# Performance work log

Hardware: AMD Instinct MI355X
Metric: run time of the kernel (lower is better)

Reference implementation:

```python
import jax, jax.numpy as jnp
import numpy as np

D_MODEL = 2048
NUM_GROUPS = 16
D_HEAD = D_MODEL // NUM_GROUPS
ROTARY_DIM = int(D_MODEL * 0.25)  # 512


def setup_inputs() -> dict:
    key = jax.random.key(0)
    ks = jax.random.split(key, 8)
    B, S, N = 4, 2048, 2048
    scale = 1.0 / np.sqrt(D_MODEL)
    return {
        "query": jax.random.normal(ks[0], (B, S, D_MODEL), jnp.float32),
        "key": jax.random.normal(ks[1], (B, N, D_MODEL), jnp.float32),
        "value": jax.random.normal(ks[2], (B, N, D_MODEL), jnp.float32),
        "mask": jax.random.randint(ks[3], (B, S), 0, 2, jnp.int32),
        "position_ids": jnp.arange(S, dtype=jnp.int64) if jax.config.jax_enable_x64 else jnp.arange(S, dtype=jnp.int32),
        "Wq": jax.random.normal(ks[4], (D_MODEL, D_MODEL), jnp.float32) * scale,
        "Wk": jax.random.normal(ks[5], (D_MODEL, D_MODEL), jnp.float32) * scale,
        "Wv": jax.random.normal(ks[6], (D_MODEL, D_MODEL), jnp.float32) * scale,
        "Wo": jax.random.normal(ks[7], (D_MODEL, D_MODEL), jnp.float32) * scale,
    }


def _apply_rope_query_only(q, k, position_ids):
    # Faithful to source: rotary embedding is applied to query ONLY; key is returned unchanged.
    rd = ROTARY_DIM
    pos = position_ids.astype(q.dtype)  # (S,)
    freq = jnp.arange(0, rd, 2, dtype=q.dtype)
    inv_freq = 1.0 / (10000.0 ** (freq / rd))  # (rd/2,)
    pe = pos[:, None] * inv_freq[None, :]       # (S, rd/2)
    cos = jnp.tile(jnp.cos(pe), (1, 2))[None]   # (1, S, rd) tiled [c, c]
    sin = jnp.tile(jnp.sin(pe), (1, 2))[None]
    q_rot, q_pass = q[..., :rd], q[..., rd:]
    half = rd // 2
    q_rot_half = jnp.concatenate([-q_rot[..., half:], q_rot[..., :half]], axis=-1)
    q_rot = q_rot * cos + q_rot_half * sin
    q = jnp.concatenate([q_rot, q_pass], axis=-1)
    return q, k


def reference(query, key, value, mask, position_ids, Wq, Wk, Wv, Wo):
    B, S, _ = query.shape
    N = key.shape[1]
    G, dh = NUM_GROUPS, D_HEAD

    q = query @ Wq.T
    k = key @ Wk.T
    v = value @ Wv.T

    q, k = _apply_rope_query_only(q, k, position_ids)

    qh = q.reshape(B, S, G, dh).transpose(0, 2, 1, 3)  # (B,G,S,dh)
    kh = k.reshape(B, N, G, dh).transpose(0, 2, 1, 3)  # (B,G,N,dh)
    vh = v.reshape(B, N, G, dh).transpose(0, 2, 1, 3)  # (B,G,N,dh)

    scores = jnp.einsum("bgsd,bgnd->bgsn", qh, kh) / jnp.sqrt(jnp.asarray(dh, q.dtype))
    # mask (B,S) -> (B,1,1,N); here S == N so pad width is 0 (pad value 1 in source)
    m = mask[:, None, None, :]
    scores = jnp.where(m == 0, -jnp.inf, scores)

    w = jax.nn.softmax(scores, axis=-1)
    out = jnp.einsum("bgsn,bgnd->bgsd", w, vh)           # (B,G,S,dh)
    out = out.transpose(0, 2, 1, 3).reshape(B, S, D_MODEL)
    return out @ Wo.T
```

## Files before the change

### kernel.cpp

```cpp
#include <hip/hip_runtime.h>
#include <hip/hip_bf16.h>
#include <type_traits>
#include <utility>

typedef unsigned short u16;
typedef unsigned int u32;
typedef __attribute__((ext_vector_type(8))) short  s16x8;
typedef __attribute__((ext_vector_type(4))) short  s16x4;
typedef __attribute__((ext_vector_type(4))) float  f32x4;
typedef __attribute__((ext_vector_type(16))) float f32x16;
typedef __bf16 bf16x8_t __attribute__((ext_vector_type(8)));
typedef __bf16 bf16x2_t __attribute__((ext_vector_type(2)));

#define SEQ 2048
#define DMODEL 2048
#define NBATCH 4
#define DH 128
#define NB (NBATCH * SEQ)

#define QK_SCALE_LOG2 0.12754375f
#define BIAS_VALID  (-34.624681f)
#define BIAS_MASKED (-180.0f)

#if __has_builtin(__builtin_amdgcn_exp2f)
#define EXP2(x) __builtin_amdgcn_exp2f(x)
#else
#define EXP2(x) exp2f(x)
#endif

#define BARRIER __builtin_amdgcn_s_barrier()
#define LGKM0  asm volatile("s_waitcnt lgkmcnt(0)" ::: "memory")
#define VMCNT4 asm volatile("s_waitcnt vmcnt(4)" ::: "memory")
#define VMCNT0 asm volatile("s_waitcnt vmcnt(0)" ::: "memory")

static __device__ __forceinline__ u16 f2bf(float f) {
  unsigned u = __float_as_uint(f);
  u += 0x7fffu + ((u >> 16) & 1u);
  return (u16)(u >> 16);
}
static __device__ __forceinline__ float bf2f(u16 h) {
  return __uint_as_float(((unsigned)h) << 16);
}
static __device__ __forceinline__ u32 pack_bf16(float a, float b) {
  bf16x2_t t; t[0] = (__bf16)a; t[1] = (__bf16)b;
  return __builtin_bit_cast(u32, t);
}
static __device__ __forceinline__ void plswap(u32& a, u32& b) {
  asm("v_permlane32_swap_b32 %0, %1" : "+v"(a), "+v"(b));
}

template <typename T, typename = void>
struct mfma_takes : std::false_type {};
template <typename T>
struct mfma_takes<T, std::void_t<decltype(__builtin_amdgcn_mfma_f32_16x16x32_bf16(
    std::declval<T>(), std::declval<T>(), std::declval<f32x4>(), 0, 0, 0))>>
    : std::true_type {};
using mfma_frag_t = std::conditional_t<mfma_takes<s16x8>::value, s16x8, bf16x8_t>;

static __device__ __forceinline__ f32x16 mfma32(s16x8 a, s16x8 b, f32x16 c) {
  return __builtin_amdgcn_mfma_f32_32x32x16_bf16(
      __builtin_bit_cast(mfma_frag_t, a), __builtin_bit_cast(mfma_frag_t, b), c, 0, 0, 0);
}

typedef const void __attribute__((address_space(1)))* gas_ptr;
typedef void __attribute__((address_space(3)))* las_ptr;
static __device__ __forceinline__ void gload16(const void* g, void* l) {
  __builtin_amdgcn_global_load_lds((gas_ptr)g, (las_ptr)l, 16, 0, 0);
}

static __device__ __forceinline__ s16x8 frag_from_words(u32 w0, u32 w1, u32 w2, u32 w3) {
  union { u32 w[4]; s16x8 v; } u;
  u.w[0] = w0; u.w[1] = w1; u.w[2] = w2; u.w[3] = w3;
  return u.v;
}

static __device__ __forceinline__ void cvt8(const float* src, u16* dst, int i) {
  const float4* p = (const float4*)src + (size_t)i * 2;
  float4 a = p[0], b4 = p[1];
  s16x8 o;
  o[0] = (short)f2bf(a.x);  o[1] = (short)f2bf(a.y);
  o[2] = (short)f2bf(a.z);  o[3] = (short)f2bf(a.w);
  o[4] = (short)f2bf(b4.x); o[5] = (short)f2bf(b4.y);
  o[6] = (short)f2bf(b4.z); o[7] = (short)f2bf(b4.w);
  *(s16x8*)(dst + (size_t)i * 8) = o;
}

__global__ void cvtall_k(const float* __restrict__ q, const float* __restrict__ a,
                         const float* __restrict__ b, const float* __restrict__ c,
                         const float* __restrict__ d, u16* __restrict__ oq,
                         u16* __restrict__ oa, u16* __restrict__ ob,
                         u16* __restrict__ oc, u16* __restrict__ od) {
  const int nq = 1 << 21, nw = 1 << 19;
  const int total = nq + 4 * nw;
  const int stride = (int)(gridDim.x * blockDim.x);
  for (int i = (int)(blockIdx.x * blockDim.x + threadIdx.x); i < total; i += stride) {
    if (i < nq) {
      cvt8(q, oq, i);
    } else {
      const int j = i - nq;
      const int seg = j >> 19, off = j & (nw - 1);
      const float* src = seg == 0 ? a : (seg == 1 ? b : (seg == 2 ? c : d));
      u16* dst = seg == 0 ? oa : (seg == 1 ? ob : (seg == 2 ? oc : od));
      cvt8(src, dst, off);
    }
  }
}

__global__ void scan_k(const int* __restrict__ mask, int* __restrict__ idx,
                       u16* __restrict__ biasc, int* __restrict__ meta) {
  __shared__ int nv_sh[4];
  const int tid = (int)threadIdx.x;
  const int w = tid >> 6, lane = tid & 63;
  const int* mb = mask + w * SEQ;
  int cnt = 0;
  for (int it = 0; it < SEQ / 64; ++it) {
    const int i = it * 64 + lane;
    const bool m = mb[i] != 0;
    const unsigned long long bal = __ballot(m);
    const int pos = cnt + __popcll(bal & ((1ull << lane) - 1ull));
    if (m) idx[w * SEQ + pos] = i;
    cnt += __popcll(bal);
  }
  if (lane == 0) nv_sh[w] = cnt;
  __syncthreads();
  const int nv = nv_sh[w];
  const int npad = (nv + 255) & ~255;
  for (int j = nv + lane; j < npad; j += 64) idx[w * SEQ + j] = 0;
  for (int j = lane; j < SEQ; j += 64)
    biasc[w * SEQ + j] = (j < nv) ? f2bf(BIAS_VALID) : f2bf(BIAS_MASKED);
  if (tid == 0) {
    int off = 0;
    for (int b2 = 0; b2 < 4; ++b2) {
      const int nvb = nv_sh[b2];
      meta[b2] = off;
      meta[4 + b2] = (nvb + 63) >> 6;
      off += (nvb + 255) & ~255;
    }
    meta[8] = off;
  }
}

__global__ void gathercvt_k(const float* __restrict__ keyf,
                            const float* __restrict__ valf,
                            const int* __restrict__ idx, const int* __restrict__ meta,
                            u16* __restrict__ xkc, u16* __restrict__ xvc) {
  const int b = (int)blockIdx.y;
  const int j = (int)blockIdx.x;
  const int mstart = meta[b];
  const int mend = (b < 3) ? meta[b + 1] : meta[8];
  if (mstart + j >= mend) return;
  const int src = idx[b * SEQ + j];
  const float* ks = keyf + ((size_t)b * SEQ + src) * DMODEL;
  const float* vs = valf + ((size_t)b * SEQ + src) * DMODEL;
  u16* kd = xkc + (size_t)(mstart + j) * DMODEL;
  u16* vd = xvc + (size_t)(mstart + j) * DMODEL;
  cvt8(ks, kd, (int)threadIdx.x);
  cvt8(vs, vd, (int)threadIdx.x);
}

static __device__ void gemm_body(const u16* __restrict__ A, const u16* __restrict__ Bw,
                                 void* __restrict__ Cv, const int outmode,
                                 const int bm, const int bn, const int mlimit) {
  constexpr int M = 8192, N = 2048, K = 2048;
  constexpr int NT = K / 64;
  __shared__ u16 Ab[2][256 * 64];
  __shared__ u16 Bb[2][256 * 64];

  if (bm * 256 >= mlimit) return;

  const int tid = (int)threadIdx.x;
  const int wv = tid >> 6, lane = tid & 63;
  const int l32 = lane & 31, hi = lane >> 5;
  const int wm = wv >> 2, wn = wv & 3;

  const size_t arow0 = (size_t)bm * 256;
  const size_t brow0 = (size_t)bn * 256;

  const int srow = tid >> 3;
  const int scolb = (tid & 7) * 16;
  const int scol = (scolb ^ ((srow & 7) << 4)) >> 1;
  const u16* agp = A  + (arow0 + srow) * (size_t)K + scol;
  const u16* bgp = Bw + (brow0 + srow) * (size_t)K + scol;

  f32x16 acc[4][2];
#pragma unroll
  for (int mi = 0; mi < 4; ++mi)
#pragma unroll
    for (int ni = 0; ni < 2; ++ni)
#pragma unroll
      for (int r = 0; r < 16; ++r) acc[mi][ni][r] = 0.f;

  auto SH_A = [&](int kt2, u16* bufA, int half) {
#pragma unroll
    for (int j = 0; j < 2; ++j) {
      const int rb = half * 128 + j * 64;
      gload16(agp + (size_t)rb * K + kt2, bufA + (rb + wv * 8) * 64);
    }
  };
  auto SH_B = [&](int kt2, u16* bufB, int half) {
#pragma unroll
    for (int j = 0; j < 2; ++j) {
      const int rb = half * 128 + j * 64;
      gload16(bgp + (size_t)rb * K + kt2, bufB + (rb + wv * 8) * 64);
    }
  };
  auto LDA = [&](const u16* buf, int qm, s16x8* af) {
#pragma unroll
    for (int mb = 0; mb < 2; ++mb) {
      const int row = wm * 128 + qm * 64 + mb * 32 + l32;
#pragma unroll
      for (int ks = 0; ks < 4; ++ks) {
        const int cb = ((ks * 32 + hi * 16) ^ ((row & 7) << 4)) >> 1;
        af[mb * 4 + ks] = *(const s16x8*)&buf[row * 64 + cb];
      }
    }
  };
  auto LDB = [&](const u16* buf, int qn, s16x8* bfr) {
    const int row = wn * 64 + qn * 32 + l32;
#pragma unroll
    for (int ks = 0; ks < 4; ++ks) {
      const int cb = ((ks * 32 + hi * 16) ^ ((row & 7) << 4)) >> 1;
      bfr[ks] = *(const s16x8*)&buf[row * 64 + cb];
    }
  };
  auto MM = [&](const s16x8* af, const s16x8* bfr, int qm, int qn) {
    __builtin_amdgcn_s_setprio(1);
#pragma unroll
    for (int mb = 0; mb < 2; ++mb)
#pragma unroll
      for (int ks = 0; ks < 4; ++ks)
        acc[qm * 2 + mb][qn] = mfma32(af[mb * 4 + ks], bfr[ks], acc[qm * 2 + mb][qn]);
    __builtin_amdgcn_s_setprio(0);
  };

  SH_A(0, Ab[0], 0); SH_A(0, Ab[0], 1);
  SH_B(0, Bb[0], 0); SH_B(0, Bb[0], 1);
  SH_B(64, Bb[1], 0); SH_B(64, Bb[1], 1);
  VMCNT4; BARRIER;

  for (int t = 0; t < NT; ++t) {
    u16* Ac = Ab[t & 1];
    u16* Bc = Bb[t & 1];
    u16* An = Ab[(t + 1) & 1];
    u16* Bn = Bb[t & 1];
    const int kA = (t + 1) * 64;
    const int kB = (t + 2) * 64;
    const bool stA = (t + 1 < NT);
    const bool stB = (t + 2 < NT);
    s16x8 af0[8], af1[8], bf0[4], bf1[4];

    LDA(Ac, 0, af0); LDB(Bc, 0, bf0);
    if (stA) SH_A(kA, An, 0);
    BARRIER; LGKM0;
    MM(af0, bf0, 0, 0);
    BARRIER;
    LDB(Bc, 1, bf1);
    if (stA) SH_A(kA, An, 1);
    BARRIER; LGKM0;
    MM(af0, bf1, 0, 1);
    BARRIER;
    LDA(Ac, 1, af1);
    if (stB) SH_B(kB, Bn, 0);
    BARRIER; LGKM0;
    MM(af1, bf1, 1, 1);
    BARRIER;
    if (stB) { SH_B(kB, Bn, 1); VMCNT4; }
    else if (stA) { VMCNT0; }
    BARRIER; LGKM0;
    MM(af1, bf0, 1, 0);
    BARRIER;
  }

  const size_t row0 = arow0 + (size_t)wm * 128;
  const size_t col0 = brow0 + (size_t)wn * 64;
  if (outmode == 0) {
    u16* C = (u16*)Cv;
#pragma unroll
    for (int mi = 0; mi < 4; ++mi)
#pragma unroll
      for (int ni = 0; ni < 2; ++ni) {
        const size_t rbase = row0 + mi * 32 + 4 * hi;
        const size_t c = col0 + ni * 32 + l32;
#pragma unroll
        for (int q = 0; q < 4; ++q)
#pragma unroll
          for (int rr = 0; rr < 4; ++rr)
            C[(rbase + 8 * q + rr) * N + c] = f2bf(acc[mi][ni][q * 4 + rr]);
      }
  } else if (outmode == 1) {
    float* C = (float*)Cv;
#pragma unroll
    for (int mi = 0; mi < 4; ++mi)
#pragma unroll
      for (int ni = 0; ni < 2; ++ni) {
        const size_t rbase = row0 + mi * 32 + 4 * hi;
        const size_t c = col0 + ni * 32 + l32;
#pragma unroll
        for (int q = 0; q < 4; ++q)
#pragma unroll
          for (int rr = 0; rr < 4; ++rr)
            C[(rbase + 8 * q + rr) * N + c] = acc[mi][ni][q * 4 + rr];
      }
  } else {
    u16* T = &Ab[0][0];
    constexpr int RS = 264;
    u16* C = (u16*)Cv;
    for (int c = 0; c < 4; ++c) {
      BARRIER;
      if (wn == c) {
#pragma unroll
        for (int mi = 0; mi < 4; ++mi)
#pragma unroll
          for (int ni = 0; ni < 2; ++ni) {
            const int tok0 = wm * 128 + mi * 32 + 4 * hi;
            const int dc = ni * 32 + l32;
#pragma unroll
            for (int q = 0; q < 4; ++q) {
              s16x4 v;
#pragma unroll
              for (int rr = 0; rr < 4; ++rr) v[rr] = (short)f2bf(acc[mi][ni][q * 4 + rr]);
              *(s16x4*)&T[dc * RS + tok0 + 8 * q] = v;
            }
          }
      }
      BARRIER;
      const int dr = tid >> 3, tc = tid & 7;
      u16* dst = C + (brow0 + c * 64 + dr) * (size_t)M + arow0 + tc * 32;
      const u16* srcT = &T[dr * RS + tc * 32];
#pragma unroll
      for (int v4 = 0; v4 < 4; ++v4)
        *(s16x8*)(dst + v4 * 8) = *(const s16x8*)(srcT + v4 * 8);
    }
    BARRIER;
  }
}

__global__ __launch_bounds__(512, 2) void gemmfused_k(
    const u16* __restrict__ xq, const u16* __restrict__ wq, u16* __restrict__ qout,
    const u16* __restrict__ xkc, const u16* __restrict__ wk, u16* __restrict__ kout,
    const u16* __restrict__ xvc, const u16* __restrict__ wv, u16* __restrict__ vtout,
    const int* __restrict__ meta) {
  const int bid = (int)blockIdx.x;
  const int gb = bid & 255;
  const int bn = (gb >> 3) & 7;
  const int bm = (gb & 7) * 4 + (gb >> 6);
  if (bid >= 256) {
    gemm_body(xq, wq, (void*)qout, 0, bm, bn, 8192);
  } else {
    const int mc = meta[8];
    gemm_body(xkc, wk, (void*)kout, 0, bm, bn, mc);
    gemm_body(xvc, wv, (void*)vtout, 2, 31 - bm, bn, mc);
  }
}

__global__ __launch_bounds__(512, 2) void gemmwo_k(const u16* __restrict__ A,
                                                   const u16* __restrict__ Bw,
                                                   float* __restrict__ C) {
  const int bid = (int)blockIdx.x;
  const int bn = (bid >> 3) & 7;
  const int bm = (bid & 7) * 4 + (bid >> 6);
  gemm_body(A, Bw, (void*)C, 1, bm, bn, 8192);
}

__global__ void rope_k(u16* __restrict__ qb, const int* __restrict__ pos_ids) {
  const int row = (int)blockIdx.x;
  const int s = row & (SEQ - 1);
  const int t = (int)threadIdx.x;
  const float pos = (float)pos_ids[s];
  const float ang = pos * exp2f((float)t * (-13.287712379549449f / 256.0f));
  float sn, cs;
  sincosf(ang, &sn, &cs);
  u16* p = qb + (size_t)row * DMODEL;
  const float x = bf2f(p[t]);
  const float y = bf2f(p[t + 256]);
  p[t]       = f2bf((x * cs - y * sn) * QK_SCALE_LOG2);
  p[t + 256] = f2bf((y * cs + x * sn) * QK_SCALE_LOG2);
#pragma unroll
  for (int j = 0; j < 6; ++j) {
    const int d = 512 + t + 256 * j;
    p[d] = f2bf(bf2f(p[d]) * QK_SCALE_LOG2);
  }
}

__device__ __forceinline__ void attn_stage(u16* Ks, u16* Vs,
                                           const u16* kbase, const u16* vbase,
                                           int kt, int w, int lane) {
#pragma unroll
  for (int i = 0; i < 4; ++i) {
    const int row = w * 16 + i * 4 + (lane >> 4);
    const int srcb = ((lane & 15) * 16) ^ ((row & 7) << 4);
    gload16(kbase + (size_t)(kt + row) * DMODEL + (srcb >> 1), &Ks[(w * 16 + i * 4) * 128]);
  }
#pragma unroll
  for (int i = 0; i < 4; ++i) {
    const int row = w * 32 + i * 8 + (lane >> 3);
    const int srcb = ((lane & 7) * 16) ^ ((row & 7) << 4);
    gload16(vbase + (size_t)row * NB + kt + (srcb >> 1), &Vs[(w * 32 + i * 8) * 64]);
  }
}

__global__ __launch_bounds__(256) void attn_k(const u16* __restrict__ q,
                                              const u16* __restrict__ kc,
                                              const u16* __restrict__ vtc,
                                              const u16* __restrict__ biasc,
                                              const int* __restrict__ meta,
                                              u16* __restrict__ att) {
  __shared__ u16 Ks[2][64 * 128];
  __shared__ u16 Vs[2][128 * 64];

  const int tid = (int)threadIdx.x;
  const int w = tid >> 6, lane = tid & 63;
  const int l32 = lane & 31, hi = lane >> 5;

  const int bid = (int)blockIdx.x;
  const int sb = (bid & 7) * 128 + (bid >> 3);
  const int qt = sb & 15;
  const int bg = sb >> 4;
  const int b = bg >> 4, g = bg & 15;

  const int mstart = meta[b];
  const int nt = meta[4 + b];

  const int qrow = qt * 128 + w * 32 + l32;
  const u16* qp = q + ((size_t)b * SEQ + qrow) * DMODEL + g * DH;
  s16x8 aq[8];
#pragma unroll
  for (int s = 0; s < 8; ++s) aq[s] = *(const s16x8*)(qp + s * 16 + hi * 8);

  const u32 one0 = (hi == 0) ? 0x00003F80u : 0u;
  const s16x8 bones = frag_from_words(one0, 0, 0, 0);
  const s16x8 allones = frag_from_words(0x3F803F80u, 0x3F803F80u, 0x3F803F80u, 0x3F803F80u);

  f32x16 oacc[4], lacc;
#pragma unroll
  for (int r = 0; r < 16; ++r) {
    lacc[r] = 0.f;
#pragma unroll
    for (int d0 = 0; d0 < 4; ++d0) oacc[d0][r] = 0.f;
  }

  const u16* kbase = kc + (size_t)mstart * DMODEL + g * DH;
  const u16* vbase = vtc + (size_t)(g * DH) * NB + mstart;
  const u16* bbase = biasc + b * SEQ;

  attn_stage(Ks[0], Vs[0], kbase, vbase, 0, w, lane);
  u16 bb0 = bbase[l32], bb1 = bbase[32 + l32];

  for (int t = 0; t < nt; ++t) {
    const int cur = t & 1;
    __syncthreads();
    u16 bbn0 = bb0, bbn1 = bb1;
    if (t < nt - 1) {
      attn_stage(Ks[cur ^ 1], Vs[cur ^ 1], kbase, vbase, (t + 1) * 64, w, lane);
      bbn0 = bbase[(t + 1) * 64 + l32];
      bbn1 = bbase[(t + 1) * 64 + 32 + l32];
    }
    const u16* KsC = Ks[cur];
    const u16* VsC = Vs[cur];

    const s16x8 ab0 = frag_from_words((hi == 0) ? (u32)bb0 : 0u, 0, 0, 0);
    const s16x8 ab1 = frag_from_words((hi == 0) ? (u32)bb1 : 0u, 0, 0, 0);
    __builtin_amdgcn_s_setprio(1);
    f32x16 sacc0 = mfma32(ab0, bones, (f32x16)(0.f));
    f32x16 sacc1 = mfma32(ab1, bones, (f32x16)(0.f));

#pragma unroll
    for (int s = 0; s < 8; ++s) {
      const int byteoff = ((s * 32 + hi * 16) ^ ((l32 & 7) << 4)) >> 1;
      const s16x8 a0 = *(const s16x8*)&KsC[l32 * 128 + byteoff];
      const s16x8 a1 = *(const s16x8*)&KsC[(32 + l32) * 128 + byteoff];
      sacc0 = mfma32(a0, aq[s], sacc0);
      sacc1 = mfma32(a1, aq[s], sacc1);
    }
    __builtin_amdgcn_s_setprio(0);

    u32 pk0[8], pk1[8];
#pragma unroll
    for (int i = 0; i < 8; ++i) {
      pk0[i] = pack_bf16(EXP2(sacc0[2 * i]), EXP2(sacc0[2 * i + 1]));
      pk1[i] = pack_bf16(EXP2(sacc1[2 * i]), EXP2(sacc1[2 * i + 1]));
    }
    s16x8 pa[4];
#pragma unroll
    for (int grp = 0; grp < 4; ++grp) {
      u32* pk = (grp < 2) ? pk0 : pk1;
      const int o = (grp & 1) * 4;
      plswap(pk[o + 0], pk[o + 2]);
      plswap(pk[o + 1], pk[o + 3]);
      pa[grp] = frag_from_words(pk[o + 0], pk[o + 1], pk[o + 2], pk[o + 3]);
    }

    __builtin_amdgcn_s_setprio(1);
#pragma unroll
    for (int ks = 0; ks < 4; ++ks) lacc = mfma32(pa[ks], allones, lacc);

#pragma unroll
    for (int d0 = 0; d0 < 4; ++d0) {
      const int rowd = d0 * 32 + l32;
#pragma unroll
      for (int ks = 0; ks < 4; ++ks) {
        const int byteoff = ((ks * 32 + hi * 16) ^ ((rowd & 7) << 4)) >> 1;
        const s16x8 bv = *(const s16x8*)&VsC[rowd * 64 + byteoff];
        oacc[d0] = mfma32(pa[ks], bv, oacc[d0]);
      }
    }
    __builtin_amdgcn_s_setprio(0);
    bb0 = bbn0; bb1 = bbn1;
  }

  float rinv[16];
#pragma unroll
  for (int r = 0; r < 16; ++r) rinv[r] = 1.0f / lacc[r];
  u16* ob = att + ((size_t)b * SEQ + qt * 128 + w * 32) * DMODEL + g * DH;
#pragma unroll
  for (int d0 = 0; d0 < 4; ++d0)
#pragma unroll
    for (int r = 0; r < 16; ++r) {
      const int qloc = (r & 3) + 8 * (r >> 2) + 4 * hi;
      ob[(size_t)qloc * DMODEL + d0 * 32 + l32] = f2bf(oacc[d0][r] * rinv[r]);
    }
}

extern "C" void kernel_launch(void* const* d_in, const int* in_sizes, int n_in,
                              void* d_out, int out_size, void* d_ws, size_t ws_size,
                              hipStream_t stream) {
  const float* query = (const float*)d_in[0];
  const float* key   = (const float*)d_in[1];
  const float* value = (const float*)d_in[2];
  const int*   maskp = (const int*)d_in[3];
  const int*   posp  = (const int*)d_in[4];
  const float* Wq    = (const float*)d_in[5];
  const float* Wk    = (const float*)d_in[6];
  const float* Wv    = (const float*)d_in[7];
  const float* Wo    = (const float*)d_in[8];

  char* ws = (char*)d_ws;
  const size_t MB = 1024ull * 1024ull;
  u16* wq_b = (u16*)(ws + 0 * MB);
  u16* wk_b = (u16*)(ws + 8 * MB);
  u16* wv_b = (u16*)(ws + 16 * MB);
  u16* wo_b = (u16*)(ws + 24 * MB);
  u16* xq   = (u16*)(ws + 32 * MB);
  u16* xkc  = (u16*)(ws + 64 * MB);
  u16* xvc  = (u16*)(ws + 96 * MB);
  u16* qb   = (u16*)(ws + 128 * MB);
  u16* kc   = (u16*)(ws + 160 * MB);
  u16* vtc  = (u16*)(ws + 192 * MB);
  char* aux = ws + 224 * MB;
  int* meta  = (int*)aux;
  int* idx   = (int*)(aux + 256);
  u16* biasc = (u16*)(aux + 256 + 32768);
  u16* att   = xq;

  scan_k<<<dim3(1), dim3(256), 0, stream>>>(maskp, idx, biasc, meta);
  cvtall_k<<<dim3(3072), dim3(256), 0, stream>>>(query, Wq, Wk, Wv, Wo,
                                                 xq, wq_b, wk_b, wv_b, wo_b);
  gathercvt_k<<<dim3(SEQ, NBATCH), dim3(256), 0, stream>>>(key, value, idx, meta, xkc, xvc);

  gemmfused_k<<<dim3(512), dim3(512), 0, stream>>>(xq, wq_b, qb, xkc, wk_b, kc,
                                                   xvc, wv_b, vtc, meta);

  rope_k<<<dim3(NBATCH * SEQ), dim3(256), 0, stream>>>(qb, posp);

  attn_k<<<dim3(1024), dim3(256), 0, stream>>>(qb, kc, vtc, biasc, meta, att);

  gemmwo_k<<<dim3(256), dim3(512), 0, stream>>>(att, wo_b, (float*)d_out);

  (void)in_sizes; (void)n_in; (void)out_size; (void)ws_size;
}
```

Baseline: 524.4 us.

## Use atomic work queue for fused QKV GEMM tiles with mask-aware job count

Replaces the fixed 512-block grid, where each K/V block ran two GEMM tiles serially, with a persistent 256-block kernel that pulls tiles from a global atomic counter. The job count for K and V is derived from the compacted (unmasked) row count, so only active tiles are scheduled and load balances dynamically across CUs. Adds a memset and per-job atomic plus two block barriers, and tile order for K/V changes, which may affect cache locality.

New measurement: 523.9 us. No clear change (-0.1%).

```diff
diff --git a/kernel.cpp b/kernel.cpp
--- a/kernel.cpp
+++ b/kernel.cpp
@@ -335,21 +335,32 @@
   }
 }
 
-__global__ __launch_bounds__(512, 2) void gemmfused_k(
+__global__ __launch_bounds__(512, 2) void gemmqkv_k(
     const u16* __restrict__ xq, const u16* __restrict__ wq, u16* __restrict__ qout,
     const u16* __restrict__ xkc, const u16* __restrict__ wk, u16* __restrict__ kout,
     const u16* __restrict__ xvc, const u16* __restrict__ wv, u16* __restrict__ vtout,
-    const int* __restrict__ meta) {
-  const int bid = (int)blockIdx.x;
-  const int gb = bid & 255;
-  const int bn = (gb >> 3) & 7;
-  const int bm = (gb & 7) * 4 + (gb >> 6);
-  if (bid >= 256) {
-    gemm_body(xq, wq, (void*)qout, 0, bm, bn, 8192);
-  } else {
-    const int mc = meta[8];
-    gemm_body(xkc, wk, (void*)kout, 0, bm, bn, mc);
-    gemm_body(xvc, wv, (void*)vtout, 2, 31 - bm, bn, mc);
+    const int* __restrict__ meta, u32* __restrict__ ctr) {
+  __shared__ int job_sh;
+  const int Mc = meta[8];
+  const int nact = (Mc >> 8) * 8;
+  const int njobs = 256 + 2 * nact;
+  for (;;) {
+    if (threadIdx.x == 0) job_sh = (int)atomicAdd(ctr, 1u);
+    __syncthreads();
+    const int j = job_sh;
+    __syncthreads();
+    if (j >= njobs) return;
+    if (j < 256) {
+      const int bn = (j >> 3) & 7;
+      const int bm = (j & 7) * 4 + (j >> 6);
+      gemm_body(xq, wq, (void*)qout, 0, bm, bn, 8192);
+    } else if (j < 256 + nact) {
+      const int g = j - 256;
+      gemm_body(xkc, wk, (void*)kout, 0, g >> 3, g & 7, Mc);
+    } else {
+      const int g = j - 256 - nact;
+      gemm_body(xvc, wv, (void*)vtout, 2, g >> 3, g & 7, Mc);
+    }
   }
 }
 
@@ -550,15 +561,17 @@
   int* meta  = (int*)aux;
   int* idx   = (int*)(aux + 256);
   u16* biasc = (u16*)(aux + 256 + 32768);
+  u32* ctr   = (u32*)(aux + 256 + 32768 + 16384);
   u16* att   = xq;
 
+  hipMemsetAsync(ctr, 0, 4, stream);
   scan_k<<<dim3(1), dim3(256), 0, stream>>>(maskp, idx, biasc, meta);
   cvtall_k<<<dim3(3072), dim3(256), 0, stream>>>(query, Wq, Wk, Wv, Wo,
                                                  xq, wq_b, wk_b, wv_b, wo_b);
   gathercvt_k<<<dim3(SEQ, NBATCH), dim3(256), 0, stream>>>(key, value, idx, meta, xkc, xvc);
 
-  gemmfused_k<<<dim3(512), dim3(512), 0, stream>>>(xq, wq_b, qb, xkc, wk_b, kc,
-                                                   xvc, wv_b, vtc, meta);
+  gemmqkv_k<<<dim3(256), dim3(512), 0, stream>>>(xq, wq_b, qb, xkc, wk_b, kc,
+                                                 xvc, wv_b, vtc, meta, ctr);
 
   rope_k<<<dim3(NBATCH * SEQ), dim3(256), 0, stream>>>(qb, posp);
 
```
